# Performance work log

Hardware: AMD Instinct MI355X
Metric: run time of the kernel (lower is better)

Reference implementation:

```python
import jax, jax.numpy as jnp
import numpy as np

E, TOPK = 32, 2            # hardcoded in LossMOEDecoder
D, HID, BOT, OUT = 768, 2048, 256, 768
B, S = 2, 128


def setup_inputs() -> dict:
    key = jax.random.key(0)
    ks = jax.random.split(key, 7)
    p = lambda k, shape: jax.random.normal(k, shape, dtype=jnp.float32) * 0.02
    return {
        "x": jax.random.normal(ks[0], (B, S, D), dtype=jnp.float32),
        "gate_w": p(ks[1], (E, D)),                 # MoEGate.weight
        "W1": p(ks[2], (E, D, HID)),  "b1": jnp.zeros((E, HID), jnp.float32),
        "W2": p(ks[3], (E, HID, HID)), "b2": jnp.zeros((E, HID), jnp.float32),
        "W3": p(ks[4], (E, HID, BOT)), "b3": jnp.zeros((E, BOT), jnp.float32),
        "Wl": p(ks[5], (E, BOT, OUT)), "bl": jnp.zeros((E, OUT), jnp.float32),
    }


def reference(x, gate_w, W1, b1, W2, b2, W3, b3, Wl, bl):
    Bz, Sl, d = x.shape
    xt = x.reshape(-1, d)                                    # [N, d] tokens
    # --- gate: softmax then top-k (values permutation-invariant vs torch sorted=False)
    scores = jax.nn.softmax(xt @ gate_w.T, axis=-1)          # [N, E]
    topk_w, topk_idx = jax.lax.top_k(scores, TOPK)           # [N, k]
    topk_w = topk_w / (topk_w.sum(-1, keepdims=True) + 1e-20)  # norm_topk_prob
    # --- experts: batched over the (small, fixed) expert axis; exact GELU as nn.GELU
    gelu = lambda v: jax.nn.gelu(v, approximate=False)
    h = gelu(jnp.einsum('nd,edh->enh', xt, W1) + b1[:, None, :])   # [E, N, HID]
    h = gelu(jnp.einsum('enh,ehg->eng', h, W2) + b2[:, None, :])   # [E, N, HID]
    z = jnp.einsum('eng,egb->enb', h, W3) + b3[:, None, :]         # [E, N, BOT]
    out_all = jnp.einsum('enb,ebo->eno', z, Wl) + bl[:, None, :]   # [E, N, OUT]
    # --- combine: gather each token's top-k expert outputs, weighted sum
    sel = jnp.take_along_axis(out_all.transpose(1, 0, 2),          # [N, E, OUT]
                              topk_idx[:, :, None], axis=1)        # [N, k, OUT]
    y = (sel * topk_w[:, :, None]).sum(axis=1)                     # [N, OUT]
    return y.reshape(Bz, Sl, OUT)
```

## Files before the change

### kernel.cpp

```cpp
#include <hip/hip_runtime.h>
#include <math.h>

#define NEXP 32
#define NTOK 256
#define DIMD 768
#define DHID 2048
#define DBOT 256
#define DOUT 768
#define NSLOT 512

__global__ __launch_bounds__(64) void gate_kernel(
    const float* __restrict__ x, const float* __restrict__ gw,
    int* __restrict__ topk_idx, float* __restrict__ topk_w) {
  const int n = blockIdx.x;
  const int l = threadIdx.x;
  const float* xr = x + n * DIMD;
  float xs[12];
#pragma unroll
  for (int j = 0; j < 12; j++) xs[j] = xr[l + 64 * j];
  float logit[NEXP];
#pragma unroll
  for (int e = 0; e < NEXP; e++) {
    const float* g = gw + e * DIMD;
    float p = 0.f;
#pragma unroll
    for (int j = 0; j < 12; j++) p = fmaf(xs[j], g[l + 64 * j], p);
#pragma unroll
    for (int m = 1; m < 64; m <<= 1) p += __shfl_xor(p, m);
    logit[e] = p;
  }
  int i0 = 0; float m0 = logit[0];
#pragma unroll
  for (int e = 1; e < NEXP; e++) { if (logit[e] > m0) { m0 = logit[e]; i0 = e; } }
  int i1 = -1; float m1 = -3.4e38f;
#pragma unroll
  for (int e = 0; e < NEXP; e++) { if (e != i0 && logit[e] > m1) { m1 = logit[e]; i1 = e; } }
  const float e1 = expf(m1 - m0);
  const float w0 = 1.f / (1.f + e1);
  const float w1 = e1 * w0;
  if (l == 0) {
    topk_idx[2 * n] = i0; topk_idx[2 * n + 1] = i1;
    topk_w[2 * n] = w0;  topk_w[2 * n + 1] = w1;
  }
}

__global__ __launch_bounds__(256) void build_lists(
    const int* __restrict__ topk_idx,
    int* __restrict__ counts, int* __restrict__ offsets,
    int* __restrict__ tok_list, int* __restrict__ tok2slot) {
  __shared__ int cnt[NEXP], base[NEXP], fill[NEXP];
  const int t = threadIdx.x;
  if (t < NEXP) { cnt[t] = 0; fill[t] = 0; }
  __syncthreads();
  const int e0 = topk_idx[2 * t], e1 = topk_idx[2 * t + 1];
  atomicAdd(&cnt[e0], 1);
  atomicAdd(&cnt[e1], 1);
  __syncthreads();
  if (t == 0) { int s = 0; for (int i = 0; i < NEXP; i++) { base[i] = s; s += cnt[i]; } }
  __syncthreads();
  const int p0 = atomicAdd(&fill[e0], 1);
  tok_list[base[e0] + p0] = t; tok2slot[2 * t] = base[e0] + p0;
  const int p1 = atomicAdd(&fill[e1], 1);
  tok_list[base[e1] + p1] = t; tok2slot[2 * t + 1] = base[e1] + p1;
  if (t < NEXP) { counts[t] = cnt[t]; offsets[t] = base[t]; }
}

__device__ __forceinline__ float gelu_f(float v) {
  return 0.5f * v * (1.f + erff(v * 0.70710678118654752f));
}

#define FMA4(A, XS, WV) \
  A.x = fmaf(XS, WV.x, A.x); A.y = fmaf(XS, WV.y, A.y); \
  A.z = fmaf(XS, WV.z, A.z); A.w = fmaf(XS, WV.w, A.w)
#define ADD4(Q, P) Q.x += P.x; Q.y += P.y; Q.z += P.z; Q.w += P.w

template <int MODE>
__global__ __launch_bounds__(256) void ff_kernel(
    const float* __restrict__ Ain, const float* __restrict__ W,
    const float* __restrict__ Bias, float* __restrict__ Out,
    const float* __restrict__ zpart,
    const int* __restrict__ offsets, const int* __restrict__ counts,
    const int* __restrict__ tok_list) {
  constexpr int NCT   = (MODE <= 1) ? 2048 : (MODE == 2) ? 256 : 768;
  constexpr int KFULL = (MODE == 0) ? 768 : (MODE == 3) ? 256 : 2048;
  constexpr int INS   = (MODE == 0) ? DIMD : DHID;
  constexpr int NSEC  = (MODE == 0) ? 12 : (MODE == 1) ? 32 : 4;
  __shared__ float Wlds[2 * 64 * 256];
  __shared__ float act_t[2 * 64 * 32];
  const int tid  = threadIdx.x;
  const int lane = tid & 63;
  const int wave = tid >> 6;
  const int e    = blockIdx.y;
  const int kb   = (MODE == 2) ? blockIdx.x : 0;
  const int ct   = (MODE == 2) ? 0 : blockIdx.x;
  const int kbase = kb * 256;
  const int cnt = counts[e];
  const int off = offsets[e];
  const int col = ct * 256 + lane * 4;
  const float* Wsrc = W + (size_t)e * KFULL * NCT + (size_t)ct * 256;
  const int tok  = tid & 31;
  const int kseg = tid >> 5;

  for (int tc0 = 0; tc0 < cnt; tc0 += 32) {
    const int tcn = min(32, cnt - tc0);
    const int slot = off + tc0 + tok;
    const float* Arow = nullptr;
    if (tok < tcn && MODE != 3) {
      const int row = (MODE == 0) ? tok_list[slot] : slot;
      Arow = Ain + (size_t)row * INS + kbase;
    }

    float4 acc[8];
#pragma unroll
    for (int t = 0; t < 8; t++) acc[t] = {0.f, 0.f, 0.f, 0.f};
    float4 av0 = {0.f, 0.f, 0.f, 0.f}, av1 = {0.f, 0.f, 0.f, 0.f};

    auto a_issue = [&](int s) {
      const int base = s * 64 + kseg * 8;
      if (MODE == 3) {
        if (tok < tcn) {
          float4 q0 = *(const float4*)(Bias + (size_t)e * DBOT + base);
          float4 q1 = *(const float4*)(Bias + (size_t)e * DBOT + base + 4);
#pragma unroll
          for (int k = 0; k < 8; k++) {
            const float* zp = zpart + ((size_t)k * NSLOT + slot) * DBOT + base;
            const float4 p0 = *(const float4*)(zp);
            const float4 p1 = *(const float4*)(zp + 4);
            ADD4(q0, p0); ADD4(q1, p1);
          }
          av0 = q0; av1 = q1;
        } else {
          av0 = {0.f, 0.f, 0.f, 0.f}; av1 = {0.f, 0.f, 0.f, 0.f};
        }
      } else {
        if (Arow) {
          av0 = *(const float4*)(Arow + base);
          av1 = *(const float4*)(Arow + base + 4);
        } else {
          av0 = {0.f, 0.f, 0.f, 0.f}; av1 = {0.f, 0.f, 0.f, 0.f};
        }
      }
    };
    auto w_issue = [&](int b, int s) {
      float* wl = Wlds + b * 16384;
      const float* src = Wsrc + (size_t)(kbase + s * 64) * NCT;
#pragma unroll
      for (int c = 0; c < 16; c++) {
        const int r = c * 4 + wave;
        __builtin_amdgcn_global_load_lds(
            (const __attribute__((address_space(1))) void*)(src + (size_t)r * NCT + lane * 4),
            (__attribute__((address_space(3))) void*)(wl + r * 256),
            16, 0, 0);
      }
    };
    auto a_write = [&](int b) {
      float* at = act_t + b * 2048;
      at[(kseg * 8 + 0) * 32 + tok] = av0.x;
      at[(kseg * 8 + 1) * 32 + tok] = av0.y;
      at[(kseg * 8 + 2) * 32 + tok] = av0.z;
      at[(kseg * 8 + 3) * 32 + tok] = av0.w;
      at[(kseg * 8 + 4) * 32 + tok] = av1.x;
      at[(kseg * 8 + 5) * 32 + tok] = av1.y;
      at[(kseg * 8 + 6) * 32 + tok] = av1.z;
      at[(kseg * 8 + 7) * 32 + tok] = av1.w;
    };

    a_issue(0);
    w_issue(0, 0);
    a_write(0);
    __syncthreads();

    for (int s = 0; s < NSEC; s++) {
      const int b = s & 1;
      if (s + 1 < NSEC) {
        a_issue(s + 1);
        w_issue(b ^ 1, s + 1);
      }
      {
        const float* wl = Wlds + b * 16384 + lane * 4;
        const float* at = act_t + b * 2048 + wave * 8;
#pragma unroll 8
        for (int r = 0; r < 64; r++) {
          const float4 wv = *(const float4*)(wl + r * 256);
          const float4 x0 = *(const float4*)(at + r * 32);
          const float4 x1 = *(const float4*)(at + r * 32 + 4);
          FMA4(acc[0], x0.x, wv);
          FMA4(acc[1], x0.y, wv);
          FMA4(acc[2], x0.z, wv);
          FMA4(acc[3], x0.w, wv);
          FMA4(acc[4], x1.x, wv);
          FMA4(acc[5], x1.y, wv);
          FMA4(acc[6], x1.z, wv);
          FMA4(acc[7], x1.w, wv);
        }
      }
      if (s + 1 < NSEC) a_write(b ^ 1);
      __syncthreads();
    }

    float4 bv = {0.f, 0.f, 0.f, 0.f};
    if (MODE <= 1) bv = *(const float4*)(Bias + (size_t)e * NCT + col);
#pragma unroll
    for (int tt = 0; tt < 8; tt++) {
      if (wave * 8 + tt < tcn) {
        const int os = off + tc0 + wave * 8 + tt;
        float4 o = acc[tt];
        if (MODE <= 1) {
          o.x = gelu_f(o.x + bv.x); o.y = gelu_f(o.y + bv.y);
          o.z = gelu_f(o.z + bv.z); o.w = gelu_f(o.w + bv.w);
          *(float4*)(Out + (size_t)os * NCT + col) = o;
        } else if (MODE == 2) {
          *(float4*)(Out + ((size_t)kb * NSLOT + os) * DBOT + lane * 4) = o;
        } else {
          *(float4*)(Out + (size_t)os * DOUT + col) = o;
        }
      }
    }
    __syncthreads();
  }
}

__global__ __launch_bounds__(192) void combine_kernel(
    const float* __restrict__ OutS, const float* __restrict__ bl,
    const int* __restrict__ topk_idx, const float* __restrict__ topk_w,
    const int* __restrict__ tok2slot, float* __restrict__ y) {
  const int n = blockIdx.x;
  const int c = threadIdx.x * 4;
  const int s0 = tok2slot[2 * n], s1 = tok2slot[2 * n + 1];
  const int e0 = topk_idx[2 * n], e1 = topk_idx[2 * n + 1];
  const float w0 = topk_w[2 * n], w1 = topk_w[2 * n + 1];
  const float4 a  = *(const float4*)(OutS + (size_t)s0 * DOUT + c);
  const float4 b  = *(const float4*)(OutS + (size_t)s1 * DOUT + c);
  const float4 ba = *(const float4*)(bl + (size_t)e0 * DOUT + c);
  const float4 bb = *(const float4*)(bl + (size_t)e1 * DOUT + c);
  float4 o;
  o.x = w0 * (a.x + ba.x) + w1 * (b.x + bb.x);
  o.y = w0 * (a.y + ba.y) + w1 * (b.y + bb.y);
  o.z = w0 * (a.z + ba.z) + w1 * (b.z + bb.z);
  o.w = w0 * (a.w + ba.w) + w1 * (b.w + bb.w);
  *(float4*)(y + (size_t)n * DOUT + c) = o;
}

extern "C" void kernel_launch(void* const* d_in, const int* in_sizes, int n_in,
                              void* d_out, int out_size, void* d_ws, size_t ws_size,
                              hipStream_t stream) {
  const float* x  = (const float*)d_in[0];
  const float* gw = (const float*)d_in[1];
  const float* W1 = (const float*)d_in[2];
  const float* b1 = (const float*)d_in[3];
  const float* W2 = (const float*)d_in[4];
  const float* b2 = (const float*)d_in[5];
  const float* W3 = (const float*)d_in[6];
  const float* b3 = (const float*)d_in[7];
  const float* Wl = (const float*)d_in[8];
  const float* bl = (const float*)d_in[9];
  float* y  = (float*)d_out;
  float* ws = (float*)d_ws;

  float* topk_w   = ws;
  int*   topk_idx = (int*)(ws + 512);
  int*   counts   = (int*)(ws + 1024);
  int*   offsets  = (int*)(ws + 1056);
  int*   tok_list = (int*)(ws + 1088);
  int*   tok2slot = (int*)(ws + 1600);
  float* B1    = ws + 4096;
  float* B2    = B1 + (size_t)NSLOT * DHID;
  float* zpart = B2 + (size_t)NSLOT * DHID;
  float* OutS  = zpart + (size_t)8 * NSLOT * DBOT;

  gate_kernel<<<NTOK, 64, 0, stream>>>(x, gw, topk_idx, topk_w);
  build_lists<<<1, 256, 0, stream>>>(topk_idx, counts, offsets, tok_list, tok2slot);
  ff_kernel<0><<<dim3(8, 32), 256, 0, stream>>>(x,  W1, b1, B1, nullptr,
                                                offsets, counts, tok_list);
  ff_kernel<1><<<dim3(8, 32), 256, 0, stream>>>(B1, W2, b2, B2, nullptr,
                                                offsets, counts, tok_list);
  ff_kernel<2><<<dim3(8, 32), 256, 0, stream>>>(B2, W3, nullptr, zpart, nullptr,
                                                offsets, counts, tok_list);
  ff_kernel<3><<<dim3(3, 32), 256, 0, stream>>>(nullptr, Wl, b3, OutS, zpart,
                                                offsets, counts, tok_list);
  combine_kernel<<<NTOK, 192, 0, stream>>>(OutS, bl, topk_idx, topk_w, tok2slot, y);
}
```

Measured before the change: 460.6 us.

## Broadcast activations via readlane and double block size in expert FF kernels

Drops the transposed activation tile in LDS. Each lane now loads one activation element per token and broadcasts it with readlane inside the inner loop. Blocks grow from 4 to 8 waves, with 4 tokens per wave instead of 8, and each wave issues half as many weight row loads into LDS. The intent is to remove LDS traffic and bank pressure for activations and to raise occupancy. In exchange, weight reuse per wave is halved, readlane instructions are added, and activation loads become scalar per-element instead of float4.

```diff
diff --git a/kernel.cpp b/kernel.cpp
--- a/kernel.cpp
+++ b/kernel.cpp
@@ -69,13 +69,16 @@
   return 0.5f * v * (1.f + erff(v * 0.70710678118654752f));
 }
 
+__device__ __forceinline__ float lane_bc(float v, int r) {
+  return __int_as_float(__builtin_amdgcn_readlane(__float_as_int(v), r));
+}
+
 #define FMA4(A, XS, WV) \
   A.x = fmaf(XS, WV.x, A.x); A.y = fmaf(XS, WV.y, A.y); \
   A.z = fmaf(XS, WV.z, A.z); A.w = fmaf(XS, WV.w, A.w)
-#define ADD4(Q, P) Q.x += P.x; Q.y += P.y; Q.z += P.z; Q.w += P.w
 
 template <int MODE>
-__global__ __launch_bounds__(256) void ff_kernel(
+__global__ __launch_bounds__(512, 2) void ff_kernel(
     const float* __restrict__ Ain, const float* __restrict__ W,
     const float* __restrict__ Bias, float* __restrict__ Out,
     const float* __restrict__ zpart,
@@ -86,7 +89,6 @@
   constexpr int INS   = (MODE == 0) ? DIMD : DHID;
   constexpr int NSEC  = (MODE == 0) ? 12 : (MODE == 1) ? 32 : 4;
   __shared__ float Wlds[2 * 64 * 256];
-  __shared__ float act_t[2 * 64 * 32];
   const int tid  = threadIdx.x;
   const int lane = tid & 63;
   const int wave = tid >> 6;
@@ -98,112 +100,96 @@
   const int off = offsets[e];
   const int col = ct * 256 + lane * 4;
   const float* Wsrc = W + (size_t)e * KFULL * NCT + (size_t)ct * 256;
-  const int tok  = tid & 31;
-  const int kseg = tid >> 5;
 
   for (int tc0 = 0; tc0 < cnt; tc0 += 32) {
     const int tcn = min(32, cnt - tc0);
-    const int slot = off + tc0 + tok;
-    const float* Arow = nullptr;
-    if (tok < tcn && MODE != 3) {
-      const int row = (MODE == 0) ? tok_list[slot] : slot;
-      Arow = Ain + (size_t)row * INS + kbase;
+    const float* Arow[4];
+    int slots[4];
+#pragma unroll
+    for (int t = 0; t < 4; t++) {
+      const int tt = wave * 4 + t;
+      slots[t] = off + tc0 + tt;
+      if (tt < tcn && MODE != 3) {
+        const int row = (MODE == 0) ? tok_list[slots[t]] : slots[t];
+        Arow[t] = Ain + (size_t)row * INS + kbase;
+      } else {
+        Arow[t] = nullptr;
+      }
     }
 
-    float4 acc[8];
-#pragma unroll
-    for (int t = 0; t < 8; t++) acc[t] = {0.f, 0.f, 0.f, 0.f};
-    float4 av0 = {0.f, 0.f, 0.f, 0.f}, av1 = {0.f, 0.f, 0.f, 0.f};
-
-    auto a_issue = [&](int s) {
-      const int base = s * 64 + kseg * 8;
+    float4 acc[4];
+#pragma unroll
+    for (int t = 0; t < 4; t++) acc[t] = {0.f, 0.f, 0.f, 0.f};
+
+    auto a_load = [&](int s, float4& dst) {
+      const int c = s * 64 + lane;
+      float q[4];
       if (MODE == 3) {
-        if (tok < tcn) {
-          float4 q0 = *(const float4*)(Bias + (size_t)e * DBOT + base);
-          float4 q1 = *(const float4*)(Bias + (size_t)e * DBOT + base + 4);
-#pragma unroll
-          for (int k = 0; k < 8; k++) {
-            const float* zp = zpart + ((size_t)k * NSLOT + slot) * DBOT + base;
-            const float4 p0 = *(const float4*)(zp);
-            const float4 p1 = *(const float4*)(zp + 4);
-            ADD4(q0, p0); ADD4(q1, p1);
-          }
-          av0 = q0; av1 = q1;
-        } else {
-          av0 = {0.f, 0.f, 0.f, 0.f}; av1 = {0.f, 0.f, 0.f, 0.f};
+#pragma unroll
+        for (int t = 0; t < 4; t++) {
+          if (wave * 4 + t < tcn) {
+            float v = Bias[(size_t)e * DBOT + c];
+#pragma unroll
+            for (int k = 0; k < 8; k++)
+              v += zpart[((size_t)k * NSLOT + slots[t]) * DBOT + c];
+            q[t] = v;
+          } else q[t] = 0.f;
         }
       } else {
-        if (Arow) {
-          av0 = *(const float4*)(Arow + base);
-          av1 = *(const float4*)(Arow + base + 4);
-        } else {
-          av0 = {0.f, 0.f, 0.f, 0.f}; av1 = {0.f, 0.f, 0.f, 0.f};
-        }
-      }
+#pragma unroll
+        for (int t = 0; t < 4; t++) q[t] = Arow[t] ? Arow[t][c] : 0.f;
+      }
+      dst = {q[0], q[1], q[2], q[3]};
     };
     auto w_issue = [&](int b, int s) {
       float* wl = Wlds + b * 16384;
       const float* src = Wsrc + (size_t)(kbase + s * 64) * NCT;
 #pragma unroll
-      for (int c = 0; c < 16; c++) {
-        const int r = c * 4 + wave;
+      for (int c = 0; c < 8; c++) {
+        const int r = c * 8 + wave;
         __builtin_amdgcn_global_load_lds(
             (const __attribute__((address_space(1))) void*)(src + (size_t)r * NCT + lane * 4),
             (__attribute__((address_space(3))) void*)(wl + r * 256),
             16, 0, 0);
       }
     };
-    auto a_write = [&](int b) {
-      float* at = act_t + b * 2048;
-      at[(kseg * 8 + 0) * 32 + tok] = av0.x;
-      at[(kseg * 8 + 1) * 32 + tok] = av0.y;
-      at[(kseg * 8 + 2) * 32 + tok] = av0.z;
-      at[(kseg * 8 + 3) * 32 + tok] = av0.w;
-      at[(kseg * 8 + 4) * 32 + tok] = av1.x;
-      at[(kseg * 8 + 5) * 32 + tok] = av1.y;
-      at[(kseg * 8 + 6) * 32 + tok] = av1.z;
-      at[(kseg * 8 + 7) * 32 + tok] = av1.w;
-    };
-
-    a_issue(0);
+
+    float4 av, av_next;
+    a_load(0, av);
     w_issue(0, 0);
-    a_write(0);
     __syncthreads();
 
     for (int s = 0; s < NSEC; s++) {
       const int b = s & 1;
       if (s + 1 < NSEC) {
-        a_issue(s + 1);
+        a_load(s + 1, av_next);
         w_issue(b ^ 1, s + 1);
       }
       {
         const float* wl = Wlds + b * 16384 + lane * 4;
-        const float* at = act_t + b * 2048 + wave * 8;
-#pragma unroll 8
+#pragma unroll
         for (int r = 0; r < 64; r++) {
           const float4 wv = *(const float4*)(wl + r * 256);
-          const float4 x0 = *(const float4*)(at + r * 32);
-          const float4 x1 = *(const float4*)(at + r * 32 + 4);
-          FMA4(acc[0], x0.x, wv);
-          FMA4(acc[1], x0.y, wv);
-          FMA4(acc[2], x0.z, wv);
-          FMA4(acc[3], x0.w, wv);
-          FMA4(acc[4], x1.x, wv);
-          FMA4(acc[5], x1.y, wv);
-          FMA4(acc[6], x1.z, wv);
-          FMA4(acc[7], x1.w, wv);
+          const float a0 = lane_bc(av.x, r);
+          const float a1 = lane_bc(av.y, r);
+          const float a2 = lane_bc(av.z, r);
+          const float a3 = lane_bc(av.w, r);
+          FMA4(acc[0], a0, wv);
+          FMA4(acc[1], a1, wv);
+          FMA4(acc[2], a2, wv);
+          FMA4(acc[3], a3, wv);
         }
       }
-      if (s + 1 < NSEC) a_write(b ^ 1);
+      av = av_next;
       __syncthreads();
     }
 
     float4 bv = {0.f, 0.f, 0.f, 0.f};
     if (MODE <= 1) bv = *(const float4*)(Bias + (size_t)e * NCT + col);
 #pragma unroll
-    for (int tt = 0; tt < 8; tt++) {
-      if (wave * 8 + tt < tcn) {
-        const int os = off + tc0 + wave * 8 + tt;
+    for (int tt = 0; tt < 4; tt++) {
+      if (wave * 4 + tt < tcn) {
+        const int os = slots[tt];
         float4 o = acc[tt];
         if (MODE <= 1) {
           o.x = gelu_f(o.x + bv.x); o.y = gelu_f(o.y + bv.y);
@@ -216,7 +202,6 @@
         }
       }
     }
-    __syncthreads();
   }
 }
 
@@ -270,13 +255,13 @@
 
   gate_kernel<<<NTOK, 64, 0, stream>>>(x, gw, topk_idx, topk_w);
   build_lists<<<1, 256, 0, stream>>>(topk_idx, counts, offsets, tok_list, tok2slot);
-  ff_kernel<0><<<dim3(8, 32), 256, 0, stream>>>(x,  W1, b1, B1, nullptr,
-                                                offsets, counts, tok_list);
-  ff_kernel<1><<<dim3(8, 32), 256, 0, stream>>>(B1, W2, b2, B2, nullptr,
-                                                offsets, counts, tok_list);
-  ff_kernel<2><<<dim3(8, 32), 256, 0, stream>>>(B2, W3, nullptr, zpart, nullptr,
-                                                offsets, counts, tok_list);
-  ff_kernel<3><<<dim3(3, 32), 256, 0, stream>>>(nullptr, Wl, b3, OutS, zpart,
+  ff_kernel<0><<<dim3(8, 32), 512, 0, stream>>>(x,  W1, b1, B1, nullptr,
+                                                offsets, counts, tok_list);
+  ff_kernel<1><<<dim3(8, 32), 512, 0, stream>>>(B1, W2, b2, B2, nullptr,
+                                                offsets, counts, tok_list);
+  ff_kernel<2><<<dim3(8, 32), 512, 0, stream>>>(B2, W3, nullptr, zpart, nullptr,
+                                                offsets, counts, tok_list);
+  ff_kernel<3><<<dim3(3, 32), 512, 0, stream>>>(nullptr, Wl, b3, OutS, zpart,
                                                 offsets, counts, tok_list);
   combine_kernel<<<NTOK, 192, 0, stream>>>(OutS, bl, topk_idx, topk_w, tok2slot, y);
 }
```

Result: slower. 499.6 us (+8.5%).
